# Performance work log

Hardware: AMD Instinct MI355X
Metric: run time of the kernel (lower is better)

Reference implementation:

```python
import jax, jax.numpy as jnp
import numpy as np

E = 64      # encoding_size (hard-coded in MatchingNetwork)
K = 5       # processing_steps


def _cell(x, h, c, Wih, Whh, bih, bhh):
    # PyTorch LSTMCell: gates ordered i, f, g, o
    z = x @ Wih.T + h @ Whh.T + bih + bhh
    i, f, g, o = jnp.split(z, 4, axis=-1)
    c2 = jax.nn.sigmoid(f) * c + jax.nn.sigmoid(i) * jnp.tanh(g)
    h2 = jax.nn.sigmoid(o) * jnp.tanh(c2)
    return h2, c2


def _lstm_seq(xs, Wih, Whh, bih, bhh, reverse=False):
    # xs: [B, S, E] -> per-step hidden states [B, S, E]
    B = xs.shape[0]
    xs_t = jnp.swapaxes(xs, 0, 1)  # [S, B, E]
    if reverse:
        xs_t = xs_t[::-1]
    h0 = jnp.zeros((B, Wih.shape[0] // 4), xs.dtype)

    def step(carry, x_t):
        h, c = carry
        h2, c2 = _cell(x_t, h, c, Wih, Whh, bih, bhh)
        return (h2, c2), h2

    _, hs = jax.lax.scan(step, (h0, h0), xs_t)
    if reverse:
        hs = hs[::-1]
    return jnp.swapaxes(hs, 0, 1)


def setup_inputs() -> dict:
    key = jax.random.key(0)
    ks = jax.random.split(key, 16)
    B, N, k, T, L, V = 64, 20, 10, 128, 40, 32000
    support_tokens = jax.random.randint(ks[0], (B, N, k, L), 0, V)
    target_tokens = jax.random.randint(ks[1], (B, T, L), 0, V)
    emb = jax.random.normal(ks[2], (V, E), jnp.float32) * 0.1
    emb = emb.at[0].set(0.0)  # padding_idx row
    s = 1.0 / np.sqrt(E)

    def lstm_params(k1, k2, k3, k4):
        return (jax.random.uniform(k1, (4 * E, E), jnp.float32, -s, s),
                jax.random.uniform(k2, (4 * E, E), jnp.float32, -s, s),
                jax.random.uniform(k3, (4 * E,), jnp.float32, -s, s),
                jax.random.uniform(k4, (4 * E,), jnp.float32, -s, s))

    f_Wih, f_Whh, f_bih, f_bhh = lstm_params(ks[3], ks[4], ks[5], ks[6])
    gf_Wih, gf_Whh, gf_bih, gf_bhh = lstm_params(ks[7], ks[8], ks[9], ks[10])
    gb_Wih, gb_Whh, gb_bih, gb_bhh = lstm_params(ks[11], ks[12], ks[13], ks[14])
    return {
        'support_tokens': support_tokens, 'target_tokens': target_tokens,
        'emb': emb,
        'f_Wih': f_Wih, 'f_Whh': f_Whh, 'f_bih': f_bih, 'f_bhh': f_bhh,
        'gf_Wih': gf_Wih, 'gf_Whh': gf_Whh, 'gf_bih': gf_bih, 'gf_bhh': gf_bhh,
        'gb_Wih': gb_Wih, 'gb_Whh': gb_Whh, 'gb_bih': gb_bih, 'gb_bhh': gb_bhh,
    }


def reference(support_tokens, target_tokens, emb,
              f_Wih, f_Whh, f_bih, f_bhh,
              gf_Wih, gf_Whh, gf_bih, gf_bhh,
              gb_Wih, gb_Whh, gb_bih, gb_bhh):
    B, N, kk, L = support_tokens.shape
    T = target_tokens.shape[1]

    # EncodingLayer: embedding lookup + sum-pool over sentence length
    sup_enc = emb[support_tokens].sum(axis=3)   # [B, N, k, E]
    tgt_enc = emb[target_tokens].sum(axis=2)    # [B, T, E]

    # GLayer: bidirectional LSTM over flattened support, sum dirs + residual
    flat = sup_enc.reshape(B, N * kk, E)
    hf = _lstm_seq(flat, gf_Wih, gf_Whh, gf_bih, gf_bhh, reverse=False)
    hb = _lstm_seq(flat, gb_Wih, gb_Whh, gb_bih, gb_bhh, reverse=True)
    sup_emb = (hf + hb).reshape(B, N, kk, E) + sup_enc  # [B, N, k, E]

    # FLayer: K-step attention LSTM over targets
    x = tgt_enc.reshape(B * T, E)
    h = jnp.zeros_like(x)
    c = jnp.zeros_like(x)
    r = jnp.zeros_like(x)
    for _ in range(K):
        h = h + r
        h_next, c = _cell(x, h, c, f_Wih, f_Whh, f_bih, f_bhh)
        h_next = h_next + x
        scores = jnp.einsum('bte,bnke->btnk', h.reshape(B, T, E), sup_emb)
        att = jax.nn.softmax(scores.reshape(B, T, N * kk), axis=2).reshape(B, T, N, kk)
        r = jnp.einsum('btnk,bnke->bte', att, sup_emb).reshape(B * T, E)
        h = h_next
    tgt_emb = h.reshape(B, T, E)

    # Cosine-similarity attention over support set (softmax over N*k)
    num = jnp.einsum('bte,bnke->btnk', tgt_emb, sup_emb)
    tn = jnp.linalg.norm(tgt_emb, axis=-1)          # [B, T]
    sn = jnp.linalg.norm(sup_emb, axis=-1)          # [B, N, k]
    sims = num / jnp.maximum(tn[:, :, None, None] * sn[:, None, :, :], 1e-8)
    attention = jax.nn.softmax(sims.reshape(B, T, N * kk), axis=2).reshape(B, T, N, kk)
    return attention
```

## Files before the change

### kernel.cpp

```cpp
#include <hip/hip_runtime.h>

#define Bn   64
#define Tn   128
#define NKn  200
#define En   64
#define Ln   40

__device__ __forceinline__ float sigm_f(float x){ return 1.0f/(1.0f+__expf(-x)); }
__device__ __forceinline__ float tanh_f(float x){ float e=__expf(2.0f*x); return 1.0f-2.0f/(e+1.0f); }
__device__ __forceinline__ float rdl(float v, int ln){
  return __uint_as_float(__builtin_amdgcn_readlane(__float_as_uint(v), (unsigned)ln));
}

__global__ __launch_bounds__(256,1) void gemm_sup2_tgt(const int* __restrict__ sup,
                                                   const float* __restrict__ emb,
                                                   float* __restrict__ sup_enc,
                                                   const float* __restrict__ Wa, const float* __restrict__ Wb,
                                                   const float* __restrict__ ba1,const float* __restrict__ ba2,
                                                   const float* __restrict__ bb1,const float* __restrict__ bb2,
                                                   float* __restrict__ outa, float* __restrict__ outb,
                                                   const int* __restrict__ tgt,
                                                   float* __restrict__ tgt_enc){
  int tid=threadIdx.x, l=tid&63, w=tid>>6;
  if (blockIdx.x >= 800){
    int r2 = (blockIdx.x-800)*16 + (tid>>4);
    int e4 = tid & 15;
    const int* tr = tgt + (size_t)r2*Ln;
    float4 acc = {0.f,0.f,0.f,0.f};
    #pragma unroll 4
    for (int t=0;t<Ln;t++){
      int tok = tr[t];
      float4 v = ((const float4*)emb)[(size_t)tok*16 + e4];
      acc.x+=v.x; acc.y+=v.y; acc.z+=v.z; acc.w+=v.w;
    }
    ((float4*)(tgt_enc + (size_t)r2*64))[e4] = acc;
    return;
  }
  int g=tid;
  int m0 = blockIdx.x*16;
  __shared__ __attribute__((aligned(16))) float xs[16*64];
  {
    int r = tid>>4, e4 = tid&15;
    const int* tr = sup + (size_t)(m0+r)*Ln;
    float4 acc = {0.f,0.f,0.f,0.f};
    #pragma unroll 4
    for (int t=0;t<Ln;t++){
      int tok = tr[t];
      float4 v = ((const float4*)emb)[(size_t)tok*16 + e4];
      acc.x+=v.x; acc.y+=v.y; acc.z+=v.z; acc.w+=v.w;
    }
    ((float4*)&xs[r*64])[e4] = acc;
    ((float4*)(sup_enc + (size_t)(m0+r)*64))[e4] = acc;
  }
  float wa[64], wb[64];
  {
    const float4* A4=(const float4*)(Wa + (size_t)g*64);
    const float4* B4=(const float4*)(Wb + (size_t)g*64);
    #pragma unroll
    for(int q=0;q<16;q++){
      float4 va=A4[q]; wa[4*q]=va.x; wa[4*q+1]=va.y; wa[4*q+2]=va.z; wa[4*q+3]=va.w;
      float4 vb=B4[q]; wb[4*q]=vb.x; wb[4*q+1]=vb.y; wb[4*q+2]=vb.z; wb[4*q+3]=vb.w;
    }
  }
  float biasa=ba1[g]+ba2[g], biasb=bb1[g]+bb2[g];
  __syncthreads();
  #pragma unroll
  for(int r=0;r<16;r++){
    const float4* x4=(const float4*)&xs[r*64];
    float a0=biasa,a1=0.f,b0=biasb,b1=0.f;
    #pragma unroll
    for(int kc=0;kc<16;kc++){
      float4 h4=x4[kc];
      a0=fmaf(wa[4*kc+0],h4.x,a0); b0=fmaf(wb[4*kc+0],h4.x,b0);
      a1=fmaf(wa[4*kc+1],h4.y,a1); b1=fmaf(wb[4*kc+1],h4.y,b1);
      a0=fmaf(wa[4*kc+2],h4.z,a0); b0=fmaf(wb[4*kc+2],h4.z,b0);
      a1=fmaf(wa[4*kc+3],h4.w,a1); b1=fmaf(wb[4*kc+3],h4.w,b1);
    }
    outa[(size_t)(m0+r)*256+g]=a0+a1;
    outb[(size_t)(m0+r)*256+g]=b0+b1;
  }
}

__global__ __launch_bounds__(256,1) void lstm_zx(const float* __restrict__ xg_f,
                                                 const float* __restrict__ xg_b,
                                                 const float* __restrict__ Whh_f,
                                                 const float* __restrict__ Whh_b,
                                                 float* __restrict__ hf,
                                                 float* __restrict__ hb,
                                                 const float* __restrict__ tgt_enc,
                                                 const float* __restrict__ Wz,
                                                 const float* __restrict__ zb1,
                                                 const float* __restrict__ zb2,
                                                 float* __restrict__ zxp){
  int tid=threadIdx.x, l=tid&63, w=tid>>6;
  if (blockIdx.x < 128){
    __builtin_amdgcn_s_setprio(1);
    int dir=blockIdx.x>>6, b=blockIdx.x&63;
    const float* xg = dir? xg_b : xg_f;
    const float* Whh= dir? Whh_b: Whh_f;
    float* out = dir? hb : hf;
    float wr[64];
    const float4* W4=(const float4*)(Whh+(size_t)(w*64+l)*64);
    #pragma unroll
    for(int q=0;q<16;q++){ float4 v=W4[q]; wr[4*q]=v.x; wr[4*q+1]=v.y; wr[4*q+2]=v.z; wr[4*q+3]=v.w; }
    __shared__ float z_s[2][256];
    float h=0.f, c=0.f;
    const int tstart = dir?(NKn-1):0, dt = dir?-1:1;
    const float* xgb = xg + (size_t)b*NKn*256 + w*64 + l;
    float xv = xgb[(size_t)tstart*256];
    for(int s=0;s<NKn;s++){
      int t=tstart+s*dt;
      float xnx=0.f;
      if (s<NKn-1) xnx = xgb[(size_t)(t+dt)*256];
      float a0=xv,a1=0.f,a2=0.f,a3=0.f;
      #pragma unroll
      for(int q=0;q<16;q++){
        a0=fmaf(wr[4*q+0],rdl(h,4*q+0),a0);
        a1=fmaf(wr[4*q+1],rdl(h,4*q+1),a1);
        a2=fmaf(wr[4*q+2],rdl(h,4*q+2),a2);
        a3=fmaf(wr[4*q+3],rdl(h,4*q+3),a3);
      }
      z_s[s&1][tid]=(a0+a1)+(a2+a3);
      __syncthreads();
      float zi=z_s[s&1][l], zf=z_s[s&1][64+l], zg=z_s[s&1][128+l], zo=z_s[s&1][192+l];
      c = sigm_f(zf)*c + sigm_f(zi)*tanh_f(zg);
      h = sigm_f(zo)*tanh_f(c);
      if(w==0) out[((size_t)b*NKn+t)*64+l]=h;
      xv=xnx;
    }
  } else {
    int g=tid, m0=(blockIdx.x-128)*16;
    __shared__ __attribute__((aligned(16))) float xs2[16*64];
    #pragma unroll
    for(int q=0;q<4;q++){ int r=4*w+q; xs2[r*64+l]=tgt_enc[(size_t)(m0+r)*64+l]; }
    float wr[64];
    const float4* W4=(const float4*)(Wz + (size_t)g*64);
    #pragma unroll
    for(int q=0;q<16;q++){ float4 v=W4[q]; wr[4*q]=v.x; wr[4*q+1]=v.y; wr[4*q+2]=v.z; wr[4*q+3]=v.w; }
    float bias=zb1[g]+zb2[g];
    __syncthreads();
    #pragma unroll
    for(int r=0;r<16;r++){
      const float4* x4=(const float4*)&xs2[r*64];
      float a0=bias,a1=0.f,a2=0.f,a3=0.f;
      #pragma unroll
      for(int kc=0;kc<16;kc++){
        float4 h4=x4[kc];
        a0=fmaf(wr[4*kc+0],h4.x,a0);
        a1=fmaf(wr[4*kc+1],h4.y,a1);
        a2=fmaf(wr[4*kc+2],h4.z,a2);
        a3=fmaf(wr[4*kc+3],h4.w,a3);
      }
      zxp[(size_t)(m0+r)*256+g]=(a0+a1)+(a2+a3);
    }
  }
}

__global__ __launch_bounds__(256,2) void combine_norm(const float* __restrict__ hf,
                                                      const float* __restrict__ hb,
                                                      const float* __restrict__ sup_enc,
                                                      float* __restrict__ semb,
                                                      float* __restrict__ sn){
  int tid=threadIdx.x, l=tid&63, w=tid>>6;
  int m0=blockIdx.x*16;
  #pragma unroll
  for(int q=0;q<4;q++){
    size_t m=(size_t)m0 + w*4 + q;
    float v = hf[m*64+l] + hb[m*64+l] + sup_enc[m*64+l];
    semb[m*64+l]=v;
    float s=v*v;
    #pragma unroll
    for (int o=32;o>0;o>>=1) s += __shfl_xor(s,o,64);
    if (l==0) sn[m]=sqrtf(s);
  }
}

__global__ __launch_bounds__(256,2) void gemmz_combine(const float* __restrict__ tgt_enc,
                                                       const float* __restrict__ W,
                                                       const float* __restrict__ b1,
                                                       const float* __restrict__ b2,
                                                       float* __restrict__ zx,
                                                       const float* __restrict__ hf,
                                                       const float* __restrict__ hb,
                                                       const float* __restrict__ sup_enc,
                                                       float* __restrict__ semb,
                                                       float* __restrict__ sn){
  int tid=threadIdx.x, l=tid&63, w=tid>>6;
  int blk=blockIdx.x;
  if (blk < 512){
    int g=tid, m0=blk*16;
    __shared__ __attribute__((aligned(16))) float xs[16*64];
    #pragma unroll
    for(int q=0;q<4;q++){ int r=4*w+q; xs[r*64+l]=tgt_enc[(size_t)(m0+r)*64+l]; }
    float wr[64];
    const float4* W4=(const float4*)(W + (size_t)g*64);
    #pragma unroll
    for(int q=0;q<16;q++){ float4 v=W4[q]; wr[4*q]=v.x; wr[4*q+1]=v.y; wr[4*q+2]=v.z; wr[4*q+3]=v.w; }
    float bias=b1[g]+b2[g];
    __syncthreads();
    #pragma unroll
    for(int r=0;r<16;r++){
      const float4* x4=(const float4*)&xs[r*64];
      float a0=bias,a1=0.f,a2=0.f,a3=0.f;
      #pragma unroll
      for(int kc=0;kc<16;kc++){
        float4 h4=x4[kc];
        a0=fmaf(wr[4*kc+0],h4.x,a0);
        a1=fmaf(wr[4*kc+1],h4.y,a1);
        a2=fmaf(wr[4*kc+2],h4.z,a2);
        a3=fmaf(wr[4*kc+3],h4.w,a3);
      }
      zx[(size_t)(m0+r)*256+g]=(a0+a1)+(a2+a3);
    }
  } else {
    int m0=(blk-512)*16;
    #pragma unroll
    for(int q=0;q<4;q++){
      size_t m=(size_t)m0 + w*4 + q;
      float v = hf[m*64+l] + hb[m*64+l] + sup_enc[m*64+l];
      semb[m*64+l]=v;
      float s=v*v;
      #pragma unroll
      for (int o=32;o>0;o>>=1) s += __shfl_xor(s,o,64);
      if (l==0) sn[m]=sqrtf(s);
    }
  }
}

__global__ __launch_bounds__(256,1) void fused_K(const float* __restrict__ zx,
                                                 const float* __restrict__ Whh,
                                                 const float* __restrict__ x,
                                                 const float* __restrict__ semb,
                                                 const float* __restrict__ sn,
                                                 float* __restrict__ out){
  int tid=threadIdx.x, l=tid&63, w=tid>>6;
  int b=blockIdx.x>>3, t0=(blockIdx.x&7)*16;
  int m0=b*Tn+t0;
  int g=tid;
  bool valid = g<NKn;
  const float* sbase = semb + (size_t)b*NKn*64;
  __shared__ __attribute__((aligned(16))) float hu_s[16*64];
  __shared__ __attribute__((aligned(16))) float sbuf[16*256];
  __shared__ __attribute__((aligned(16))) float hn_s[16*64];
  __shared__ float wredA[64], wredB[64];
  float wr[64], s4f[64];
  {
    const float4* W4=(const float4*)(Whh+(size_t)g*64);
    #pragma unroll
    for(int q=0;q<16;q++){ float4 v=W4[q]; wr[4*q]=v.x; wr[4*q+1]=v.y; wr[4*q+2]=v.z; wr[4*q+3]=v.w; }
  }
  if(valid){
    const float4* sp=(const float4*)(sbase+(size_t)g*64);
    #pragma unroll
    for(int q=0;q<16;q++){ float4 v=sp[q]; s4f[4*q]=v.x; s4f[4*q+1]=v.y; s4f[4*q+2]=v.z; s4f[4*q+3]=v.w; }
  } else {
    #pragma unroll
    for(int q=0;q<64;q++) s4f[q]=0.f;
  }
  float zxr[16];
  #pragma unroll
  for(int r=0;r<16;r++) zxr[r]=zx[(size_t)(m0+r)*256+g];
  float xr[4];
  #pragma unroll
  for(int q=0;q<4;q++) xr[q]=x[(size_t)(m0+q*4+w)*64+l];
  float snr = valid ? sn[(size_t)b*NKn+g] : 1.f;
  float cq[4]={0.f,0.f,0.f,0.f};
  float scr[16], ex[16], mx[16];
  for(int k=0;k<5;k++){
    if(k==0){
      #pragma unroll
      for(int r=0;r<16;r++){ sbuf[r*256+g]=zxr[r]; scr[r]=0.f; }
    } else {
      #pragma unroll
      for(int r=0;r<16;r++){
        float z0=zxr[r], z1=0.f, sc0=0.f, sc1=0.f;
        const float4* h4p=(const float4*)&hu_s[r*64];
        #pragma unroll
        for(int kc=0;kc<16;kc++){
          float4 h4=h4p[kc];
          z0 =fmaf(wr[4*kc+0] ,h4.x,z0 ); sc0=fmaf(s4f[4*kc+0],h4.x,sc0);
          z1 =fmaf(wr[4*kc+1] ,h4.y,z1 ); sc1=fmaf(s4f[4*kc+1],h4.y,sc1);
          z0 =fmaf(wr[4*kc+2] ,h4.z,z0 ); sc0=fmaf(s4f[4*kc+2],h4.z,sc0);
          z1 =fmaf(wr[4*kc+3] ,h4.w,z1 ); sc1=fmaf(s4f[4*kc+3],h4.w,sc1);
        }
        sbuf[r*256+g]=z0+z1;
        scr[r]=sc0+sc1;
      }
    }
    __syncthreads();
    #pragma unroll
    for(int q=0;q<4;q++){
      int r=q*4+w;
      float zi=sbuf[r*256+l], zf=sbuf[r*256+64+l], zg=sbuf[r*256+128+l], zo=sbuf[r*256+192+l];
      float c=sigm_f(zf)*cq[q]+sigm_f(zi)*tanh_f(zg);
      cq[q]=c;
      hn_s[r*64+l]=sigm_f(zo)*tanh_f(c)+xr[q];
    }
    if(k<4){
      #pragma unroll
      for(int t=0;t<16;t++){
        float m = valid ? scr[t] : -1e30f;
        #pragma unroll
        for(int o=32;o>0;o>>=1) m=fmaxf(m,__shfl_xor(m,o,64));
        mx[t]=m;
      }
      if(l==0){
        #pragma unroll
        for(int t=0;t<16;t++) wredA[t*4+w]=mx[t];
      }
      __syncthreads();
      #pragma unroll
      for(int t=0;t<16;t++){
        const float4 m4=*(const float4*)&wredA[t*4];
        float gm=fmaxf(fmaxf(m4.x,m4.y),fmaxf(m4.z,m4.w));
        float e=valid?__expf(scr[t]-gm):0.f;
        ex[t]=e;
        float s=e;
        #pragma unroll
        for(int o=32;o>0;o>>=1) s+=__shfl_xor(s,o,64);
        mx[t]=s;
      }
      if(l==0){
        #pragma unroll
        for(int t=0;t<16;t++) wredB[t*4+w]=mx[t];
      }
      __syncthreads();
      #pragma unroll
      for(int t=0;t<16;t++){
        const float4 s4v=*(const float4*)&wredB[t*4];
        float tot=(s4v.x+s4v.y)+(s4v.z+s4v.w);
        ex[t]*=1.0f/tot;
      }
      if(valid){
        #pragma unroll
        for(int cg=0;cg<4;cg++)
          *(float4*)&sbuf[g*20+4*cg]=make_float4(ex[4*cg+0],ex[4*cg+1],ex[4*cg+2],ex[4*cg+3]);
      }
      __syncthreads();
      float r0=0.f,r1=0.f,r2=0.f,r3=0.f;
      #pragma unroll 8
      for(int j=0;j<NKn;j++){
        float4 a4=*(const float4*)&sbuf[j*20+w*4];
        float sv=sbase[(size_t)j*64+l];
        r0=fmaf(a4.x,sv,r0);
        r1=fmaf(a4.y,sv,r1);
        r2=fmaf(a4.z,sv,r2);
        r3=fmaf(a4.w,sv,r3);
      }
      int rb=w*4;
      hu_s[(rb+0)*64+l]=r0 + hn_s[(rb+0)*64+l];
      hu_s[(rb+1)*64+l]=r1 + hn_s[(rb+1)*64+l];
      hu_s[(rb+2)*64+l]=r2 + hn_s[(rb+2)*64+l];
      hu_s[(rb+3)*64+l]=r3 + hn_s[(rb+3)*64+l];
      __syncthreads();
    }
  }
  __syncthreads();
  float tnorm[16];
  #pragma unroll
  for(int t=0;t<16;t++){
    float v=hn_s[t*64+l];
    float s=v*v;
    #pragma unroll
    for(int o=32;o>0;o>>=1) s+=__shfl_xor(s,o,64);
    tnorm[t]=sqrtf(s);
  }
  #pragma unroll
  for(int t=0;t<16;t++){
    const float4* h4p=(const float4*)&hn_s[t*64];
    float a0=0.f,a1=0.f;
    #pragma unroll
    for(int kc=0;kc<16;kc++){
      float4 h4=h4p[kc];
      a0=fmaf(s4f[4*kc+0],h4.x,a0);
      a1=fmaf(s4f[4*kc+1],h4.y,a1);
      a0=fmaf(s4f[4*kc+2],h4.z,a0);
      a1=fmaf(s4f[4*kc+3],h4.w,a1);
    }
    scr[t]=(a0+a1) / fmaxf(tnorm[t]*snr,1e-8f);
  }
  #pragma unroll
  for(int t=0;t<16;t++){
    float m = valid ? scr[t] : -1e30f;
    #pragma unroll
    for(int o=32;o>0;o>>=1) m=fmaxf(m,__shfl_xor(m,o,64));
    mx[t]=m;
  }
  if(l==0){
    #pragma unroll
    for(int t=0;t<16;t++) wredA[t*4+w]=mx[t];
  }
  __syncthreads();
  #pragma unroll
  for(int t=0;t<16;t++){
    const float4 m4=*(const float4*)&wredA[t*4];
    float gm=fmaxf(fmaxf(m4.x,m4.y),fmaxf(m4.z,m4.w));
    float e=valid?__expf(scr[t]-gm):0.f;
    ex[t]=e;
    float s=e;
    #pragma unroll
    for(int o=32;o>0;o>>=1) s+=__shfl_xor(s,o,64);
    mx[t]=s;
  }
  if(l==0){
    #pragma unroll
    for(int t=0;t<16;t++) wredB[t*4+w]=mx[t];
  }
  __syncthreads();
  #pragma unroll
  for(int t=0;t<16;t++){
    const float4 s4v=*(const float4*)&wredB[t*4];
    float tot=(s4v.x+s4v.y)+(s4v.z+s4v.w);
    if(valid) out[((size_t)(m0+t))*NKn + g]=ex[t]*(1.0f/tot);
  }
}

extern "C" void kernel_launch(void* const* d_in, const int* in_sizes, int n_in,
                              void* d_out, int out_size, void* d_ws, size_t ws_size,
                              hipStream_t stream) {
  (void)in_sizes; (void)n_in; (void)out_size;
  const int*   sup_toks = (const int*)d_in[0];
  const int*   tgt_toks = (const int*)d_in[1];
  const float* emb      = (const float*)d_in[2];
  const float* f_Wih    = (const float*)d_in[3];
  const float* f_Whh    = (const float*)d_in[4];
  const float* f_bih    = (const float*)d_in[5];
  const float* f_bhh    = (const float*)d_in[6];
  const float* gf_Wih   = (const float*)d_in[7];
  const float* gf_Whh   = (const float*)d_in[8];
  const float* gf_bih   = (const float*)d_in[9];
  const float* gf_bhh   = (const float*)d_in[10];
  const float* gb_Wih   = (const float*)d_in[11];
  const float* gb_Whh   = (const float*)d_in[12];
  const float* gb_bih   = (const float*)d_in[13];
  const float* gb_bhh   = (const float*)d_in[14];

  float* ws = (float*)d_ws;
  float* sup_enc = ws;
  float* tgt_enc = sup_enc + 819200;
  float* bufA    = tgt_enc + 524288;
  float* bufB    = bufA    + 3276800;
  float* semb    = bufB    + 3276800;
  float* hb      = semb    + 819200;
  float* sn      = hb      + 819200;
  float* zxded   = sn      + 12800;

  bool fused = ws_size >= (size_t)(9548288 + 2097152) * sizeof(float);
  float* zx = fused ? zxded : bufA;

  float* xg_f = bufA;
  float* xg_b = bufB;

  gemm_sup2_tgt<<<1312,256,0,stream>>>(sup_toks, emb, sup_enc,
                                       gf_Wih, gb_Wih,
                                       gf_bih, gf_bhh, gb_bih, gb_bhh, xg_f, xg_b,
                                       tgt_toks, tgt_enc);
  if (fused){
    lstm_zx<<<640,256,0,stream>>>(xg_f, xg_b, gf_Whh, gb_Whh, semb , hb,
                                  tgt_enc, f_Wih, f_bih, f_bhh, zx);
    combine_norm<<<800,256,0,stream>>>(semb , hb, sup_enc, semb, sn);
  } else {
    lstm_zx<<<128,256,0,stream>>>(xg_f, xg_b, gf_Whh, gb_Whh, semb , hb,
                                  tgt_enc, f_Wih, f_bih, f_bhh, zx);
    gemmz_combine<<<1312,256,0,stream>>>(tgt_enc, f_Wih, f_bih, f_bhh, zx,
                                         semb, hb, sup_enc, semb, sn);
  }
  fused_K<<<512,256,0,stream>>>(zx, f_Whh, tgt_enc, semb, sn, (float*)d_out);
}
```

Before: 345.6 us.

## Move target input-projection GEMM into first kernel and fold combine/norm into attention kernel

The target-side input projection (zx) now runs in the target blocks of the first embedding/GEMM kernel instead of sharing a launch with the recurrent LSTM. The LSTM becomes a standalone 128-block kernel and loses its priority hint. When the workspace is large enough, the hf+hb+sup_enc combine and the support norms are computed inside each fused_K block, removing the combine_norm launch at the cost of redundant per-batch recomputation across the 8 blocks sharing a batch. The gather loops are also unrolled further. This trades overlap of the zx GEMM with the latency-bound LSTM for fewer launches and less intermediate traffic.

```diff
diff --git a/kernel.cpp b/kernel.cpp
--- a/kernel.cpp
+++ b/kernel.cpp
@@ -20,30 +20,58 @@
                                                    const float* __restrict__ bb1,const float* __restrict__ bb2,
                                                    float* __restrict__ outa, float* __restrict__ outb,
                                                    const int* __restrict__ tgt,
-                                                   float* __restrict__ tgt_enc){
+                                                   float* __restrict__ tgt_enc,
+                                                   const float* __restrict__ Wz,
+                                                   const float* __restrict__ zb1,
+                                                   const float* __restrict__ zb2,
+                                                   float* __restrict__ zxp,
+                                                   int do_zx){
   int tid=threadIdx.x, l=tid&63, w=tid>>6;
+  __shared__ __attribute__((aligned(16))) float xs[16*64];
   if (blockIdx.x >= 800){
-    int r2 = (blockIdx.x-800)*16 + (tid>>4);
-    int e4 = tid & 15;
-    const int* tr = tgt + (size_t)r2*Ln;
+    int m0t = (blockIdx.x-800)*16;
+    int r = tid>>4, e4 = tid&15;
+    const int* tr = tgt + (size_t)(m0t+r)*Ln;
     float4 acc = {0.f,0.f,0.f,0.f};
-    #pragma unroll 4
+    #pragma unroll 8
     for (int t=0;t<Ln;t++){
       int tok = tr[t];
       float4 v = ((const float4*)emb)[(size_t)tok*16 + e4];
       acc.x+=v.x; acc.y+=v.y; acc.z+=v.z; acc.w+=v.w;
     }
-    ((float4*)(tgt_enc + (size_t)r2*64))[e4] = acc;
+    ((float4*)&xs[r*64])[e4] = acc;
+    ((float4*)(tgt_enc + (size_t)(m0t+r)*64))[e4] = acc;
+    if (!do_zx) return;
+    int g=tid;
+    float wr[64];
+    const float4* W4=(const float4*)(Wz + (size_t)g*64);
+    #pragma unroll
+    for(int q=0;q<16;q++){ float4 v=W4[q]; wr[4*q]=v.x; wr[4*q+1]=v.y; wr[4*q+2]=v.z; wr[4*q+3]=v.w; }
+    float bias=zb1[g]+zb2[g];
+    __syncthreads();
+    #pragma unroll
+    for(int r2=0;r2<16;r2++){
+      const float4* x4=(const float4*)&xs[r2*64];
+      float a0=bias,a1=0.f,a2=0.f,a3=0.f;
+      #pragma unroll
+      for(int kc=0;kc<16;kc++){
+        float4 h4=x4[kc];
+        a0=fmaf(wr[4*kc+0],h4.x,a0);
+        a1=fmaf(wr[4*kc+1],h4.y,a1);
+        a2=fmaf(wr[4*kc+2],h4.z,a2);
+        a3=fmaf(wr[4*kc+3],h4.w,a3);
+      }
+      zxp[(size_t)(m0t+r2)*256+g]=(a0+a1)+(a2+a3);
+    }
     return;
   }
   int g=tid;
   int m0 = blockIdx.x*16;
-  __shared__ __attribute__((aligned(16))) float xs[16*64];
   {
     int r = tid>>4, e4 = tid&15;
     const int* tr = sup + (size_t)(m0+r)*Ln;
     float4 acc = {0.f,0.f,0.f,0.f};
-    #pragma unroll 4
+    #pragma unroll 8
     for (int t=0;t<Ln;t++){
       int tok = tr[t];
       float4 v = ((const float4*)emb)[(size_t)tok*16 + e4];
@@ -81,78 +109,45 @@
   }
 }
 
-__global__ __launch_bounds__(256,1) void lstm_zx(const float* __restrict__ xg_f,
-                                                 const float* __restrict__ xg_b,
-                                                 const float* __restrict__ Whh_f,
-                                                 const float* __restrict__ Whh_b,
-                                                 float* __restrict__ hf,
-                                                 float* __restrict__ hb,
-                                                 const float* __restrict__ tgt_enc,
-                                                 const float* __restrict__ Wz,
-                                                 const float* __restrict__ zb1,
-                                                 const float* __restrict__ zb2,
-                                                 float* __restrict__ zxp){
+__global__ __launch_bounds__(256,1) void lstm_seq(const float* __restrict__ xg_f,
+                                                  const float* __restrict__ xg_b,
+                                                  const float* __restrict__ Whh_f,
+                                                  const float* __restrict__ Whh_b,
+                                                  float* __restrict__ hf,
+                                                  float* __restrict__ hb){
   int tid=threadIdx.x, l=tid&63, w=tid>>6;
-  if (blockIdx.x < 128){
-    __builtin_amdgcn_s_setprio(1);
-    int dir=blockIdx.x>>6, b=blockIdx.x&63;
-    const float* xg = dir? xg_b : xg_f;
-    const float* Whh= dir? Whh_b: Whh_f;
-    float* out = dir? hb : hf;
-    float wr[64];
-    const float4* W4=(const float4*)(Whh+(size_t)(w*64+l)*64);
-    #pragma unroll
-    for(int q=0;q<16;q++){ float4 v=W4[q]; wr[4*q]=v.x; wr[4*q+1]=v.y; wr[4*q+2]=v.z; wr[4*q+3]=v.w; }
-    __shared__ float z_s[2][256];
-    float h=0.f, c=0.f;
-    const int tstart = dir?(NKn-1):0, dt = dir?-1:1;
-    const float* xgb = xg + (size_t)b*NKn*256 + w*64 + l;
-    float xv = xgb[(size_t)tstart*256];
-    for(int s=0;s<NKn;s++){
-      int t=tstart+s*dt;
-      float xnx=0.f;
-      if (s<NKn-1) xnx = xgb[(size_t)(t+dt)*256];
-      float a0=xv,a1=0.f,a2=0.f,a3=0.f;
-      #pragma unroll
-      for(int q=0;q<16;q++){
-        a0=fmaf(wr[4*q+0],rdl(h,4*q+0),a0);
-        a1=fmaf(wr[4*q+1],rdl(h,4*q+1),a1);
-        a2=fmaf(wr[4*q+2],rdl(h,4*q+2),a2);
-        a3=fmaf(wr[4*q+3],rdl(h,4*q+3),a3);
-      }
-      z_s[s&1][tid]=(a0+a1)+(a2+a3);
-      __syncthreads();
-      float zi=z_s[s&1][l], zf=z_s[s&1][64+l], zg=z_s[s&1][128+l], zo=z_s[s&1][192+l];
-      c = sigm_f(zf)*c + sigm_f(zi)*tanh_f(zg);
-      h = sigm_f(zo)*tanh_f(c);
-      if(w==0) out[((size_t)b*NKn+t)*64+l]=h;
-      xv=xnx;
-    }
-  } else {
-    int g=tid, m0=(blockIdx.x-128)*16;
-    __shared__ __attribute__((aligned(16))) float xs2[16*64];
-    #pragma unroll
-    for(int q=0;q<4;q++){ int r=4*w+q; xs2[r*64+l]=tgt_enc[(size_t)(m0+r)*64+l]; }
-    float wr[64];
-    const float4* W4=(const float4*)(Wz + (size_t)g*64);
-    #pragma unroll
-    for(int q=0;q<16;q++){ float4 v=W4[q]; wr[4*q]=v.x; wr[4*q+1]=v.y; wr[4*q+2]=v.z; wr[4*q+3]=v.w; }
-    float bias=zb1[g]+zb2[g];
+  int dir=blockIdx.x>>6, b=blockIdx.x&63;
+  const float* xg = dir? xg_b : xg_f;
+  const float* Whh= dir? Whh_b: Whh_f;
+  float* out = dir? hb : hf;
+  float wr[64];
+  const float4* W4=(const float4*)(Whh+(size_t)(w*64+l)*64);
+  #pragma unroll
+  for(int q=0;q<16;q++){ float4 v=W4[q]; wr[4*q]=v.x; wr[4*q+1]=v.y; wr[4*q+2]=v.z; wr[4*q+3]=v.w; }
+  __shared__ float z_s[2][256];
+  float h=0.f, c=0.f;
+  const int tstart = dir?(NKn-1):0, dt = dir?-1:1;
+  const float* xgb = xg + (size_t)b*NKn*256 + w*64 + l;
+  float xv = xgb[(size_t)tstart*256];
+  for(int s=0;s<NKn;s++){
+    int t=tstart+s*dt;
+    float xnx=0.f;
+    if (s<NKn-1) xnx = xgb[(size_t)(t+dt)*256];
+    float a0=xv,a1=0.f,a2=0.f,a3=0.f;
+    #pragma unroll
+    for(int q=0;q<16;q++){
+      a0=fmaf(wr[4*q+0],rdl(h,4*q+0),a0);
+      a1=fmaf(wr[4*q+1],rdl(h,4*q+1),a1);
+      a2=fmaf(wr[4*q+2],rdl(h,4*q+2),a2);
+      a3=fmaf(wr[4*q+3],rdl(h,4*q+3),a3);
+    }
+    z_s[s&1][tid]=(a0+a1)+(a2+a3);
     __syncthreads();
-    #pragma unroll
-    for(int r=0;r<16;r++){
-      const float4* x4=(const float4*)&xs2[r*64];
-      float a0=bias,a1=0.f,a2=0.f,a3=0.f;
-      #pragma unroll
-      for(int kc=0;kc<16;kc++){
-        float4 h4=x4[kc];
-        a0=fmaf(wr[4*kc+0],h4.x,a0);
-        a1=fmaf(wr[4*kc+1],h4.y,a1);
-        a2=fmaf(wr[4*kc+2],h4.z,a2);
-        a3=fmaf(wr[4*kc+3],h4.w,a3);
-      }
-      zxp[(size_t)(m0+r)*256+g]=(a0+a1)+(a2+a3);
-    }
+    float zi=z_s[s&1][l], zf=z_s[s&1][64+l], zg=z_s[s&1][128+l], zo=z_s[s&1][192+l];
+    c = sigm_f(zf)*c + sigm_f(zi)*tanh_f(zg);
+    h = sigm_f(zo)*tanh_f(c);
+    if(w==0) out[((size_t)b*NKn+t)*64+l]=h;
+    xv=xnx;
   }
 }
 
@@ -230,19 +225,38 @@
 __global__ __launch_bounds__(256,1) void fused_K(const float* __restrict__ zx,
                                                  const float* __restrict__ Whh,
                                                  const float* __restrict__ x,
-                                                 const float* __restrict__ semb,
+                                                 float* __restrict__ semb,
                                                  const float* __restrict__ sn,
-                                                 float* __restrict__ out){
+                                                 float* __restrict__ out,
+                                                 const float* __restrict__ hfp,
+                                                 const float* __restrict__ hbp,
+                                                 const float* __restrict__ supp,
+                                                 int cs){
   int tid=threadIdx.x, l=tid&63, w=tid>>6;
   int b=blockIdx.x>>3, t0=(blockIdx.x&7)*16;
   int m0=b*Tn+t0;
   int g=tid;
   bool valid = g<NKn;
-  const float* sbase = semb + (size_t)b*NKn*64;
+  float* sbase = semb + (size_t)b*NKn*64;
   __shared__ __attribute__((aligned(16))) float hu_s[16*64];
   __shared__ __attribute__((aligned(16))) float sbuf[16*256];
   __shared__ __attribute__((aligned(16))) float hn_s[16*64];
   __shared__ float wredA[64], wredB[64];
+  __shared__ float sn_s[NKn];
+  if (cs){
+    size_t rb0 = (size_t)b*NKn*64;
+    for (int i=0;i<50;i++){
+      int j = i*4 + w;
+      size_t idx = rb0 + (size_t)j*64 + l;
+      float v = hfp[idx] + hbp[idx] + supp[idx];
+      sbase[(size_t)j*64+l] = v;
+      float s = v*v;
+      #pragma unroll
+      for (int o=32;o>0;o>>=1) s += __shfl_xor(s,o,64);
+      if (l==0) sn_s[j] = sqrtf(s);
+    }
+    __syncthreads();
+  }
   float wr[64], s4f[64];
   {
     const float4* W4=(const float4*)(Whh+(size_t)g*64);
@@ -263,7 +277,7 @@
   float xr[4];
   #pragma unroll
   for(int q=0;q<4;q++) xr[q]=x[(size_t)(m0+q*4+w)*64+l];
-  float snr = valid ? sn[(size_t)b*NKn+g] : 1.f;
+  float snr = valid ? (cs ? sn_s[g] : sn[(size_t)b*NKn+g]) : 1.f;
   float cq[4]={0.f,0.f,0.f,0.f};
   float scr[16], ex[16], mx[16];
   for(int k=0;k<5;k++){
@@ -444,9 +458,12 @@
   float* hb      = semb    + 819200;
   float* sn      = hb      + 819200;
   float* zxded   = sn      + 12800;
-
-  bool fused = ws_size >= (size_t)(9548288 + 2097152) * sizeof(float);
-  float* zx = fused ? zxded : bufA;
+  float* hfded   = zxded   + 2097152;
+
+  int tier = (ws_size >= (size_t)12464640*sizeof(float)) ? 2
+           : (ws_size >= (size_t)11645440*sizeof(float)) ? 1 : 0;
+  float* zx = tier ? zxded : bufA;
+  float* hf = (tier==2) ? hfded : semb;
 
   float* xg_f = bufA;
   float* xg_b = bufB;
@@ -454,16 +471,20 @@
   gemm_sup2_tgt<<<1312,256,0,stream>>>(sup_toks, emb, sup_enc,
                                        gf_Wih, gb_Wih,
                                        gf_bih, gf_bhh, gb_bih, gb_bhh, xg_f, xg_b,
-                                       tgt_toks, tgt_enc);
-  if (fused){
-    lstm_zx<<<640,256,0,stream>>>(xg_f, xg_b, gf_Whh, gb_Whh, semb , hb,
-                                  tgt_enc, f_Wih, f_bih, f_bhh, zx);
-    combine_norm<<<800,256,0,stream>>>(semb , hb, sup_enc, semb, sn);
+                                       tgt_toks, tgt_enc,
+                                       f_Wih, f_bih, f_bhh, zx, tier ? 1 : 0);
+  lstm_seq<<<128,256,0,stream>>>(xg_f, xg_b, gf_Whh, gb_Whh, hf, hb);
+  if (tier==2){
+    fused_K<<<512,256,0,stream>>>(zx, f_Whh, tgt_enc, semb, nullptr, (float*)d_out,
+                                  hf, hb, sup_enc, 1);
+  } else if (tier==1){
+    combine_norm<<<800,256,0,stream>>>(hf, hb, sup_enc, semb, sn);
+    fused_K<<<512,256,0,stream>>>(zx, f_Whh, tgt_enc, semb, sn, (float*)d_out,
+                                  nullptr, nullptr, nullptr, 0);
   } else {
-    lstm_zx<<<128,256,0,stream>>>(xg_f, xg_b, gf_Whh, gb_Whh, semb , hb,
-                                  tgt_enc, f_Wih, f_bih, f_bhh, zx);
     gemmz_combine<<<1312,256,0,stream>>>(tgt_enc, f_Wih, f_bih, f_bhh, zx,
                                          semb, hb, sup_enc, semb, sn);
-  }
-  fused_K<<<512,256,0,stream>>>(zx, f_Whh, tgt_enc, semb, sn, (float*)d_out);
-}
+    fused_K<<<512,256,0,stream>>>(zx, f_Whh, tgt_enc, semb, sn, (float*)d_out,
+                                  nullptr, nullptr, nullptr, 0);
+  }
+}
```

After: 368.6 us. +6.7%, slower.
